# Kernel optimization log

Hardware: AMD Instinct MI355X
Metric: run time of the kernel (lower is better)

The kernel has to match this reference:

```python
import jax, jax.numpy as jnp
import numpy as np

DIM = 256
HEADS = 8
HD = DIM // HEADS        # head_dim = 32
WS = 8                   # window_size (Wh = Ww = 8)
NEXP = 8                 # num_experts
HID = 128                # attr_hidden_size (router hidden)
SCALE = HD ** -0.5


def _window_partition(x, ws):
    # (B, H, W, C) -> (B * H//ws * W//ws, ws, ws, C)
    B, H, W, C = x.shape
    x = x.reshape(B, H // ws, ws, W // ws, ws, C)
    return x.transpose(0, 1, 3, 2, 4, 5).reshape(-1, ws, ws, C)


def _window_reverse(w, ws, B, H, W):
    # inverse of _window_partition
    C = w.shape[-1]
    x = w.reshape(B, H // ws, W // ws, ws, ws, C)
    return x.transpose(0, 1, 3, 2, 4, 5).reshape(B, H, W, C)


def _rope2(x):
    # 2D rotary embedding over a window: x (B*, Wh, Ww, d).
    # First d/2 channels rotated by row position, last d/2 by column position.
    B, Wh, Ww, d = x.shape
    d2 = d // 2

    def angles(L, dd):
        inv = 1.0 / (10000.0 ** (jnp.arange(0, dd, 2, dtype=jnp.float32) / dd))
        return jnp.arange(L, dtype=jnp.float32)[:, None] * inv[None, :]  # (L, dd//2)

    def rotate(v, ang, bshape):
        # v: (B, Wh, Ww, dd) pairs interleaved; ang broadcast as bshape
        p = v.reshape(*v.shape[:-1], -1, 2)
        c = jnp.cos(ang).reshape(bshape)
        s = jnp.sin(ang).reshape(bshape)
        o0 = p[..., 0] * c - p[..., 1] * s
        o1 = p[..., 0] * s + p[..., 1] * c
        return jnp.stack([o0, o1], axis=-1).reshape(v.shape)

    ah = angles(Wh, d2)  # (Wh, d2//2)
    aw = angles(Ww, d2)  # (Ww, d2//2)
    xh = rotate(x[..., :d2], ah, (1, Wh, 1, d2 // 2))
    xw = rotate(x[..., d2:], aw, (1, 1, Ww, d2 // 2))
    return jnp.concatenate([xh, xw], axis=-1)


def _moe_linear(xf, routes, w, b):
    # Top-1 dispatch: per-expert dense GEMM, masked select (jit-safe, static shapes).
    # xf: (T, in), routes: (T,) int, w: (E, out, in), b: (E, out)
    out = jnp.zeros((xf.shape[0], w.shape[1]), xf.dtype)
    for i in range(w.shape[0]):
        y = xf @ w[i].T + b[i]
        out = jnp.where((routes == i)[:, None], y, out)
    return out


def setup_inputs() -> dict:
    key = jax.random.key(0)
    ks = jax.random.split(key, 8)
    sc = 0.02
    return {
        "x": jax.random.normal(ks[0], (8, 64, 64, DIM), jnp.float32),
        "router_w1": jax.random.normal(ks[1], (HID, DIM), jnp.float32) * sc,
        "router_b1": jnp.zeros((HID,), jnp.float32),
        "router_w2": jax.random.normal(ks[2], (NEXP, HID), jnp.float32) * sc,
        "router_b2": jnp.zeros((NEXP,), jnp.float32),
        "qkv_w": jax.random.normal(ks[3], (NEXP, 3 * DIM, DIM), jnp.float32) * sc,
        "qkv_b": jnp.zeros((NEXP, 3 * DIM), jnp.float32),
        "proj_w": jax.random.normal(ks[4], (NEXP, DIM, DIM), jnp.float32) * sc,
        "proj_b": jnp.zeros((NEXP, DIM), jnp.float32),
    }


def reference(x, router_w1, router_b1, router_w2, router_b2,
              qkv_w, qkv_b, proj_w, proj_b):
    Bs, H, W, C = x.shape
    xf = x.reshape(-1, C)  # (T, C), T = Bs*H*W

    # --- Top-1 router (eval mode: no noise, no token dropping) ---
    h = jax.nn.relu(xf @ router_w1.T + router_b1)
    router_logits = h @ router_w2.T + router_b2          # (T, E)
    router_probs = jax.nn.softmax(router_logits, axis=-1)
    route_prob_max = jnp.max(router_probs, axis=-1)       # (T,)
    routes = jnp.argmax(router_probs, axis=-1)            # (T,)

    # --- per-expert QKV projection (grouped dispatch) ---
    qkv = _moe_linear(xf, routes, qkv_w, qkv_b)           # (T, 3C)
    qkv = qkv.reshape(Bs, H, W, 3 * C)

    # --- window partition (shift=0, dilated=1 -> no roll, mask=None) ---
    qw = _window_partition(qkv, WS).reshape(-1, WS * WS, 3 * C)
    B_, N, _ = qw.shape
    qkv5 = qw.reshape(B_, N, 3, HEADS, HD).transpose(2, 0, 3, 1, 4)  # (3,B_,h,N,hd)
    q, k, v = qkv5[0], qkv5[1], qkv5[2]

    # --- RoPE on q, k over the 2D window ---
    q = _rope2(q.reshape(-1, WS, WS, HD)).reshape(B_, HEADS, N, HD)
    k = _rope2(k.reshape(-1, WS, WS, HD)).reshape(B_, HEADS, N, HD)

    # --- windowed attention (moe_mask is all zeros in eval: no drops) ---
    attn = jax.nn.softmax((q * SCALE) @ k.swapaxes(-2, -1), axis=-1)  # (B_,h,N,N)
    out = (attn @ v).swapaxes(1, 2).reshape(B_, N, C)

    # --- window reverse ---
    out = _window_reverse(out.reshape(-1, WS, WS, C), WS, Bs, H, W)

    # --- per-expert output projection + Switch-style prob scaling ---
    of = _moe_linear(out.reshape(-1, C), routes, proj_w, proj_b)
    of = of * route_prob_max[:, None]
    return of.reshape(Bs, H, W, C)
```

## Files before the change

kernel.cpp:

```cpp
#include <hip/hip_runtime.h>
#include <hip/hip_bf16.h>

typedef unsigned short u16;
typedef unsigned int u32;
typedef __attribute__((ext_vector_type(8))) short short8;
typedef __attribute__((ext_vector_type(4))) float f32x4;

#define T_TOK 32768
#define SCALE_ATT 0.17677669529663687f

__device__ __forceinline__ u16 f2bf(float f){
  u32 u = __float_as_uint(f);
  u32 r = u + 0x7fffu + ((u >> 16) & 1u);
  return (u16)(r >> 16);
}
__device__ __forceinline__ float bf2f(u16 h){
  return __uint_as_float(((u32)h) << 16);
}

__global__ void k_cvt(const float* __restrict__ s, u16* __restrict__ d, int n4){
  int i = blockIdx.x * blockDim.x + threadIdx.x;
  if (i < n4){
    float4 v = ((const float4*)s)[i];
    ushort4 o;
    o.x = f2bf(v.x); o.y = f2bf(v.y); o.z = f2bf(v.z); o.w = f2bf(v.w);
    ((ushort4*)d)[i] = o;
  }
}

__global__ void k_cvt_split(const float* __restrict__ s, u16* __restrict__ hi,
                            u16* __restrict__ lo, int n){
  int i = blockIdx.x * blockDim.x + threadIdx.x;
  if (i < n){
    float v = s[i];
    u16 h = f2bf(v);
    hi[i] = h;
    lo[i] = f2bf(v - bf2f(h));
  }
}

__global__ void k_init(int* counts, int* cursors){
  int t = threadIdx.x;
  if (t < 8){ counts[t] = 0; cursors[t] = 0; }
}

__global__ __launch_bounds__(256) void k_router(
    const float* __restrict__ x, const u16* __restrict__ w1h, const u16* __restrict__ w1l,
    const float* __restrict__ b1, const float* __restrict__ w2, const float* __restrict__ b2,
    int* __restrict__ routes, float* __restrict__ pmax, int* __restrict__ counts,
    u16* __restrict__ x_bf)
{
  __shared__ __align__(16) char smem[64*132*4];
  u16* Ah = (u16*)smem;
  u16* Al = Ah + 2560;
  u16* Bh = Al + 2560;
  u16* Bl = Bh + 5120;
  float* Hs = (float*)smem;
  __shared__ int lhist[8];

  int tid = threadIdx.x;
  int t0 = blockIdx.x * 64;
  int wv = tid >> 6, lane = tid & 63, quad = lane >> 4, l16 = lane & 15;
  if (tid < 8) lhist[tid] = 0;

  int arow = tid >> 2, acg = tid & 3;
  int brow = tid >> 1, bhalf = tid & 1;

  f32x4 acc[4][2];
  #pragma unroll
  for (int i = 0; i < 4; ++i)
    #pragma unroll
    for (int j = 0; j < 2; ++j)
      #pragma unroll
      for (int rr = 0; rr < 4; ++rr) acc[i][j][rr] = 0.f;

  for (int kt = 0; kt < 8; ++kt){
    const float* gx = x + (size_t)(t0 + arow) * 256 + kt * 32 + acg * 8;
    float4 v0 = *(const float4*)gx;
    float4 v1 = *(const float4*)(gx + 4);
    ushort4 h0, h1, l0, l1;
    h0.x = f2bf(v0.x); h0.y = f2bf(v0.y); h0.z = f2bf(v0.z); h0.w = f2bf(v0.w);
    h1.x = f2bf(v1.x); h1.y = f2bf(v1.y); h1.z = f2bf(v1.z); h1.w = f2bf(v1.w);
    l0.x = f2bf(v0.x - bf2f(h0.x)); l0.y = f2bf(v0.y - bf2f(h0.y));
    l0.z = f2bf(v0.z - bf2f(h0.z)); l0.w = f2bf(v0.w - bf2f(h0.w));
    l1.x = f2bf(v1.x - bf2f(h1.x)); l1.y = f2bf(v1.y - bf2f(h1.y));
    l1.z = f2bf(v1.z - bf2f(h1.z)); l1.w = f2bf(v1.w - bf2f(h1.w));
    u16* gxb = x_bf + (size_t)(t0 + arow) * 256 + kt * 32 + acg * 8;
    *(ushort4*)gxb = h0; *(ushort4*)(gxb + 4) = h1;
    const u16* gwh = w1h + (size_t)brow * 256 + kt * 32 + bhalf * 16;
    const u16* gwl = w1l + (size_t)brow * 256 + kt * 32 + bhalf * 16;
    uint4 wh0 = *(const uint4*)gwh;
    uint4 wh1 = *(const uint4*)(gwh + 8);
    uint4 wl0 = *(const uint4*)gwl;
    uint4 wl1 = *(const uint4*)(gwl + 8);
    __syncthreads();
    *(ushort4*)&Ah[arow*40 + acg*8    ] = h0;
    *(ushort4*)&Ah[arow*40 + acg*8 + 4] = h1;
    *(ushort4*)&Al[arow*40 + acg*8    ] = l0;
    *(ushort4*)&Al[arow*40 + acg*8 + 4] = l1;
    *(uint4*)&Bh[brow*40 + bhalf*16    ] = wh0;
    *(uint4*)&Bh[brow*40 + bhalf*16 + 8] = wh1;
    *(uint4*)&Bl[brow*40 + bhalf*16    ] = wl0;
    *(uint4*)&Bl[brow*40 + bhalf*16 + 8] = wl1;
    __syncthreads();
    short8 ah[4], al[4], bhf[2], blf[2];
    #pragma unroll
    for (int i = 0; i < 4; ++i){
      ah[i] = *(const short8*)&Ah[(i*16 + l16)*40 + quad*8];
      al[i] = *(const short8*)&Al[(i*16 + l16)*40 + quad*8];
    }
    #pragma unroll
    for (int j = 0; j < 2; ++j){
      bhf[j] = *(const short8*)&Bh[(wv*32 + j*16 + l16)*40 + quad*8];
      blf[j] = *(const short8*)&Bl[(wv*32 + j*16 + l16)*40 + quad*8];
    }
    #pragma unroll
    for (int i = 0; i < 4; ++i)
      #pragma unroll
      for (int j = 0; j < 2; ++j){
        acc[i][j] = __builtin_amdgcn_mfma_f32_16x16x32_bf16(ah[i], bhf[j], acc[i][j], 0, 0, 0);
        acc[i][j] = __builtin_amdgcn_mfma_f32_16x16x32_bf16(ah[i], blf[j], acc[i][j], 0, 0, 0);
        acc[i][j] = __builtin_amdgcn_mfma_f32_16x16x32_bf16(al[i], bhf[j], acc[i][j], 0, 0, 0);
      }
  }
  __syncthreads();

  #pragma unroll
  for (int i = 0; i < 4; ++i)
    #pragma unroll
    for (int j = 0; j < 2; ++j){
      int col = wv*32 + j*16 + l16;
      float bb = b1[col];
      #pragma unroll
      for (int rr = 0; rr < 4; ++rr){
        float h = acc[i][j][rr] + bb;
        Hs[(i*16 + quad*4 + rr)*132 + col] = h > 0.f ? h : 0.f;
      }
    }
  __syncthreads();

  #pragma unroll
  for (int pass = 0; pass < 2; ++pass){
    int mtok = (tid >> 3) + pass * 32;
    int e = tid & 7;
    const float4* w2r = (const float4*)(w2 + e * 128);
    float l = b2[e];
    #pragma unroll
    for (int k4 = 0; k4 < 32; ++k4){
      float4 w = w2r[k4];
      int k = k4 * 4;
      l = fmaf(Hs[mtok*132+k  ], w.x, l);
      l = fmaf(Hs[mtok*132+k+1], w.y, l);
      l = fmaf(Hs[mtok*132+k+2], w.z, l);
      l = fmaf(Hs[mtok*132+k+3], w.w, l);
    }
    float mv = l; int mi = e;
    #pragma unroll
    for (int off = 1; off < 8; off <<= 1){
      float ov = __shfl_xor(mv, off, 64);
      int   oi = __shfl_xor(mi, off, 64);
      if (ov > mv || (ov == mv && oi < mi)){ mv = ov; mi = oi; }
    }
    float sum = expf(l - mv);
    #pragma unroll
    for (int off = 1; off < 8; off <<= 1) sum += __shfl_xor(sum, off, 64);
    if (e == 0){
      int t = t0 + mtok;
      routes[t] = mi;
      pmax[t] = 1.0f / sum;
      atomicAdd(&lhist[mi], 1);
    }
  }
  __syncthreads();
  if (tid < 8 && lhist[tid] > 0) atomicAdd(&counts[tid], lhist[tid]);
}

__global__ void k_offsets(const int* __restrict__ counts, int* __restrict__ offs,
                          int* __restrict__ sorted){
  __shared__ int so[9];
  if (threadIdx.x == 0){
    int o = 0; so[0] = 0;
    for (int e = 0; e < 8; ++e){ o += ((counts[e] + 127) >> 7) << 7; so[e+1] = o; }
    for (int e = 0; e < 9; ++e) offs[e] = so[e];
  }
  __syncthreads();
  for (int e = 0; e < 8; ++e){
    int s = so[e] + counts[e], en = so[e+1];
    for (int i = s + (int)threadIdx.x; i < en; i += (int)blockDim.x) sorted[i] = -1;
  }
}

__global__ __launch_bounds__(256) void k_scatter(
    const int* __restrict__ routes, const int* __restrict__ offs,
    int* __restrict__ cursors, int* __restrict__ sorted, int* __restrict__ rank)
{
  __shared__ int lc[8], lb[8];
  int tid = threadIdx.x;
  int t = blockIdx.x * 256 + tid;
  if (tid < 8) lc[tid] = 0;
  __syncthreads();
  int e = routes[t];
  int rl = atomicAdd(&lc[e], 1);
  __syncthreads();
  if (tid < 8 && lc[tid] > 0) lb[tid] = atomicAdd(&cursors[tid], lc[tid]);
  __syncthreads();
  int pos = offs[e] + lb[e] + rl;
  sorted[pos] = t;
  rank[t] = pos;
}

__global__ __launch_bounds__(256) void k_gather(
    const u16* __restrict__ xbf, const int* __restrict__ sorted,
    const int* __restrict__ offs, u16* __restrict__ xs)
{
  int total = offs[8];
  int tid = threadIdx.x;
  #pragma unroll
  for (int h = 0; h < 2; ++h){
    int cid = tid + h * 256;
    int row = cid >> 5, chunk = cid & 31;
    int gr = blockIdx.x * 16 + row;
    int t = (gr < total) ? sorted[gr] : -1;
    uint4 v = {0u, 0u, 0u, 0u};
    if (t >= 0) v = *(const uint4*)(xbf + (size_t)t * 256 + chunk * 8);
    *(uint4*)(xs + (size_t)gr * 256 + chunk * 8) = v;
  }
}

#define ASTR 56
template<int NOUT, bool PROJ>
__global__ __launch_bounds__(256) void k_gemm(
    const u16* __restrict__ A, const u16* __restrict__ W,
    const float* __restrict__ bias, const int* __restrict__ sidx,
    const int* __restrict__ offs, const float* __restrict__ pmax,
    u16* __restrict__ outb, float* __restrict__ outf)
{
  __shared__ __align__(16) u16 As[128 * ASTR];
  __shared__ __align__(16) u16 Bs[128 * ASTR];
  int tid = threadIdx.x;
  int m0 = blockIdx.y * 128;
  int n0 = blockIdx.x * 128;
  int total = offs[8];
  if (m0 >= total) return;
  int e = 0;
  #pragma unroll
  for (int i = 1; i < 8; ++i) if (m0 >= offs[i]) e = i;

  int wv = tid >> 6, lane = tid & 63, quad = lane >> 4, l16 = lane & 15;
  int wrow = (wv >> 1) * 64, wcol = (wv & 1) * 64;

  int row0 = tid >> 2, c0 = tid & 3;
  const u16* aptr0 = A + (size_t)(m0 + row0) * 256 + c0 * 8;
  const u16* aptr1 = aptr0 + (size_t)64 * 256;
  int pc = (row0 >> 4) + (row0 & 15) * 4;
  const u16* bptr0 = W + ((size_t)e * NOUT + n0 + pc) * 256 + c0 * 8;
  const u16* bptr1 = W + ((size_t)e * NOUT + n0 + 64 + pc) * 256 + c0 * 8;

  f32x4 acc[4][4];
  #pragma unroll
  for (int i = 0; i < 4; ++i)
    #pragma unroll
    for (int j = 0; j < 4; ++j)
      #pragma unroll
      for (int r = 0; r < 4; ++r) acc[i][j][r] = 0.f;

  uint4 a0 = *(const uint4*)aptr0, a1 = *(const uint4*)aptr1;
  uint4 b0 = *(const uint4*)bptr0, b1 = *(const uint4*)bptr1;

  for (int kt = 0; kt < 8; ++kt){
    __syncthreads();
    *(uint4*)&As[ row0      *ASTR + c0*8] = a0;
    *(uint4*)&As[(row0 + 64)*ASTR + c0*8] = a1;
    *(uint4*)&Bs[ row0      *ASTR + c0*8] = b0;
    *(uint4*)&Bs[(row0 + 64)*ASTR + c0*8] = b1;
    __syncthreads();
    if (kt < 7){
      a0 = *(const uint4*)(aptr0 + (kt+1)*32);
      a1 = *(const uint4*)(aptr1 + (kt+1)*32);
      b0 = *(const uint4*)(bptr0 + (kt+1)*32);
      b1 = *(const uint4*)(bptr1 + (kt+1)*32);
    }
    short8 af[4], bfv[4];
    #pragma unroll
    for (int i = 0; i < 4; ++i)
      af[i] = *(const short8*)&As[(wrow + i*16 + l16)*ASTR + quad*8];
    #pragma unroll
    for (int j = 0; j < 4; ++j)
      bfv[j] = *(const short8*)&Bs[(wcol + j*16 + l16)*ASTR + quad*8];
    #pragma unroll
    for (int i = 0; i < 4; ++i)
      #pragma unroll
      for (int j = 0; j < 4; ++j)
        acc[i][j] = __builtin_amdgcn_mfma_f32_16x16x32_bf16(af[i], bfv[j], acc[i][j], 0, 0, 0);
  }

  float4 bj4 = *(const float4*)&bias[e*NOUT + n0 + wcol + l16*4];
  if (PROJ){
    #pragma unroll
    for (int i = 0; i < 4; ++i){
      #pragma unroll
      for (int ri = 0; ri < 4; ++ri){
        int row = wrow + i*16 + quad*4 + ri;
        int t = sidx[m0 + row];
        if (t < 0) continue;
        float pm = pmax[t];
        float4 ov;
        ov.x = (acc[i][0][ri] + bj4.x) * pm;
        ov.y = (acc[i][1][ri] + bj4.y) * pm;
        ov.z = (acc[i][2][ri] + bj4.z) * pm;
        ov.w = (acc[i][3][ri] + bj4.w) * pm;
        *(float4*)&outf[(size_t)t * NOUT + n0 + wcol + l16*4] = ov;
      }
    }
  } else {
    int col0 = n0 + wcol + l16*4;
    bool isqk = (col0 < 512);
    float inv0 = 0.f, inv1 = 0.f;
    float qsc = (col0 < 256) ? SCALE_ATT : 1.0f;
    if (isqk){
      int p0 = (col0 & 15) >> 1;
      inv0 = __expf(-1.1512925465f * (float)p0);
      inv1 = inv0 * 0.31622776601683794f;
    }
    #pragma unroll
    for (int i = 0; i < 4; ++i){
      #pragma unroll
      for (int ri = 0; ri < 4; ++ri){
        int row = wrow + i*16 + quad*4 + ri;
        int t = sidx[m0 + row];
        if (t < 0) continue;
        float vx = acc[i][0][ri] + bj4.x;
        float vy = acc[i][1][ri] + bj4.y;
        float vz = acc[i][2][ri] + bj4.z;
        float vw = acc[i][3][ri] + bj4.w;
        if (isqk){
          float pos = (float)((col0 & 16) ? (t & 7) : ((t >> 6) & 7));
          float a0 = pos * inv0, a1 = pos * inv1;
          float s0, c0s, s1, c1s;
          __sincosf(a0, &s0, &c0s);
          __sincosf(a1, &s1, &c1s);
          float r0 = (vx*c0s - vy*s0) * qsc;
          float r1 = (vx*s0 + vy*c0s) * qsc;
          float r2 = (vz*c1s - vw*s1) * qsc;
          float r3 = (vz*s1 + vw*c1s) * qsc;
          vx = r0; vy = r1; vz = r2; vw = r3;
        }
        uint2 ov;
        ov.x = (u32)f2bf(vx) | ((u32)f2bf(vy) << 16);
        ov.y = (u32)f2bf(vz) | ((u32)f2bf(vw) << 16);
        *(uint2*)&outb[(size_t)t * NOUT + n0 + wcol + l16*4] = ov;
      }
    }
  }
}

__global__ __launch_bounds__(64, 3) void k_attn(const u16* __restrict__ qkv,
                                                const int* __restrict__ rank,
                                                u16* __restrict__ attn_s)
{
  __shared__ __align__(16) u16 Ps[64*72];
  __shared__ __align__(16) u16 Vt[32*72];

  int lane = threadIdx.x;
  int quad = lane >> 4, l16 = lane & 15;
  int wh = blockIdx.x;
  int win = wh >> 3, head = wh & 7;
  int b = win >> 6, wy = (win >> 3) & 7, wx = win & 7;
  int tb = b*4096 + wy*512 + wx*8;

  short8 qf[4], kf[4];
  #pragma unroll
  for (int i = 0; i < 4; ++i){
    int n = i*16 + l16;
    const u16* p = qkv + (size_t)(tb + (n>>3)*64 + (n&7)) * 768 + head*32 + quad*8;
    qf[i] = *(const short8*)p;
    kf[i] = *(const short8*)(p + 256);
  }
  int tn = tb + (lane>>3)*64 + (lane&7);
  const uint4* vb = (const uint4*)(qkv + (size_t)tn * 768 + 512 + head*32);
  uint4 va[4];
  #pragma unroll
  for (int i = 0; i < 4; ++i) va[i] = vb[i];

  f32x4 sa[4][4];
  #pragma unroll
  for (int i = 0; i < 4; ++i)
    #pragma unroll
    for (int j = 0; j < 4; ++j){
      #pragma unroll
      for (int rr = 0; rr < 4; ++rr) sa[i][j][rr] = 0.f;
      sa[i][j] = __builtin_amdgcn_mfma_f32_16x16x32_bf16(qf[i], kf[j], sa[i][j], 0, 0, 0);
    }

  f32x4 rs[4];
  #pragma unroll
  for (int i = 0; i < 4; ++i)
    #pragma unroll
    for (int rr = 0; rr < 4; ++rr){
      float e0 = __expf(sa[i][0][rr]);
      float e1 = __expf(sa[i][1][rr]);
      float e2 = __expf(sa[i][2][rr]);
      float e3 = __expf(sa[i][3][rr]);
      rs[i][rr] = (e0 + e1) + (e2 + e3);
      uint2 pk;
      pk.x = (u32)f2bf(e0) | ((u32)f2bf(e1) << 16);
      pk.y = (u32)f2bf(e2) | ((u32)f2bf(e3) << 16);
      *(uint2*)&Ps[(i*16 + quad*4 + rr)*72 + l16*4] = pk;
    }
  #pragma unroll
  for (int i = 0; i < 4; ++i)
    #pragma unroll
    for (int rr = 0; rr < 4; ++rr){
      #pragma unroll
      for (int off = 1; off < 16; off <<= 1)
        rs[i][rr] += __shfl_xor(rs[i][rr], off, 64);
    }

  u32* vu = (u32*)va;
  int pn = l16 * 4 + quad;
  #pragma unroll
  for (int d2 = 0; d2 < 16; ++d2){
    Vt[(2*d2  )*72 + pn] = (u16)(vu[d2] & 0xffff);
    Vt[(2*d2+1)*72 + pn] = (u16)(vu[d2] >> 16);
  }

  f32x4 oa[4][2];
  #pragma unroll
  for (int i = 0; i < 4; ++i)
    #pragma unroll
    for (int rr = 0; rr < 4; ++rr){ oa[i][0][rr] = 0.f; oa[i][1][rr] = 0.f; }
  #pragma unroll
  for (int ks = 0; ks < 2; ++ks){
    short8 vf0 = *(const short8*)&Vt[(     l16)*72 + ks*32 + quad*8];
    short8 vf1 = *(const short8*)&Vt[(16 + l16)*72 + ks*32 + quad*8];
    #pragma unroll
    for (int i = 0; i < 4; ++i){
      short8 pf = *(const short8*)&Ps[(i*16 + l16)*72 + ks*32 + quad*8];
      oa[i][0] = __builtin_amdgcn_mfma_f32_16x16x32_bf16(pf, vf0, oa[i][0], 0, 0, 0);
      oa[i][1] = __builtin_amdgcn_mfma_f32_16x16x32_bf16(pf, vf1, oa[i][1], 0, 0, 0);
    }
  }

  #pragma unroll
  for (int i = 0; i < 4; ++i)
    #pragma unroll
    for (int rr = 0; rr < 4; ++rr){
      float inv = __builtin_amdgcn_rcpf(rs[i][rr]);
      int m = i*16 + quad*4 + rr;
      int tm = tb + (m >> 3) * 64 + (m & 7);
      int pos = rank[tm];
      u16* op = attn_s + (size_t)pos * 256 + head * 32 + l16;
      op[0]  = f2bf(oa[i][0][rr] * inv);
      op[16] = f2bf(oa[i][1][rr] * inv);
    }
}

extern "C" void kernel_launch(void* const* d_in, const int* in_sizes, int n_in,
                              void* d_out, int out_size, void* d_ws, size_t ws_size,
                              hipStream_t stream){
  const float* x     = (const float*)d_in[0];
  const float* rw1   = (const float*)d_in[1];
  const float* rb1   = (const float*)d_in[2];
  const float* rw2   = (const float*)d_in[3];
  const float* rb2   = (const float*)d_in[4];
  const float* qkvw  = (const float*)d_in[5];
  const float* qkvb  = (const float*)d_in[6];
  const float* projw = (const float*)d_in[7];
  const float* projb = (const float*)d_in[8];
  float* out = (float*)d_out;

  char* ws = (char*)d_ws;
  u16*   x_bf    = (u16*)(ws);
  u16*   qkv_bf  = (u16*)(ws + 16777216);
  u16*   w1h     = (u16*)(ws + 67108864);
  u16*   w1l     = w1h + 32768;
  u16*   xs      = (u16*)(ws + 67108864);
  u16*   attn_s  = (u16*)(ws + 67108864);
  u16*   qw_bf   = (u16*)(ws + 84410368);
  u16*   pw_bf   = (u16*)(ws + 87556096);
  int*   routes  = (int*)(ws + 88604672);
  float* pmaxp   = (float*)(ws + 88735744);
  int*   sorted  = (int*)(ws + 88866816);
  int*   rank    = (int*)(ws + 89001984);
  int*   counts  = (int*)(ws + 89133056);
  int*   cursors = (int*)(ws + 89133056 + 32);
  int*   offs    = (int*)(ws + 89133056 + 64);

  k_init<<<1, 64, 0, stream>>>(counts, cursors);
  k_cvt<<<1536, 256, 0, stream>>>(qkvw,  qw_bf, 1572864/4);
  k_cvt<<< 512, 256, 0, stream>>>(projw, pw_bf,  524288/4);
  k_cvt_split<<<128, 256, 0, stream>>>(rw1, w1h, w1l, 32768);
  k_router<<<512, 256, 0, stream>>>(x, w1h, w1l, rb1, rw2, rb2, routes, pmaxp, counts, x_bf);
  k_offsets<<<1, 256, 0, stream>>>(counts, offs, sorted);
  k_scatter<<<128, 256, 0, stream>>>(routes, offs, cursors, sorted, rank);
  k_gather<<<2112, 256, 0, stream>>>(x_bf, sorted, offs, xs);
  k_gemm<768, false><<<dim3(6, 264), 256, 0, stream>>>(xs, qw_bf, qkvb, sorted, offs,
                                                       nullptr, qkv_bf, nullptr);
  k_attn<<<4096, 64, 0, stream>>>(qkv_bf, rank, attn_s);
  k_gemm<256, true><<<dim3(2, 264), 256, 0, stream>>>(attn_s, pw_bf, projb, sorted, offs,
                                                      pmaxp, nullptr, out);
}
```

Baseline: 224.6 us.

## Fuse prep kernels, fold gather into QKV GEMM, add XCD-aware block swizzle

Merges the weight conversion, split, init and sorted-buffer fill kernels into one prep launch. Folds offset computation into the scatter kernel and removes the gather kernel by having the QKV GEMM load A rows indirectly through the sorted index. Adds an XCD-aware remapping of block IDs in both GEMMs and the attention kernel so neighbouring tiles land on the same chiplet's L2. This cuts launches and an intermediate copy, at the cost of non-contiguous A-row loads inside the GEMM.

```diff
diff --git a/kernel.cpp b/kernel.cpp
--- a/kernel.cpp
+++ b/kernel.cpp
@@ -18,30 +18,42 @@
   return __uint_as_float(((u32)h) << 16);
 }
 
-__global__ void k_cvt(const float* __restrict__ s, u16* __restrict__ d, int n4){
-  int i = blockIdx.x * blockDim.x + threadIdx.x;
-  if (i < n4){
-    float4 v = ((const float4*)s)[i];
+__device__ __forceinline__ int xcd_swz(int flat, int nwg){
+  return (flat & 7) * (nwg >> 3) + (flat >> 3);
+}
+
+__global__ __launch_bounds__(256) void k_prep(
+    const float* __restrict__ qkvw, u16* __restrict__ qw_bf,
+    const float* __restrict__ projw, u16* __restrict__ pw_bf,
+    const float* __restrict__ rw1, u16* __restrict__ w1h, u16* __restrict__ w1l,
+    int* __restrict__ sorted, int* __restrict__ counts, int* __restrict__ cursors)
+{
+  int b = blockIdx.x, tid = threadIdx.x;
+  if (b < 1536){
+    int i = b * 256 + tid;
+    float4 v = ((const float4*)qkvw)[i];
     ushort4 o;
     o.x = f2bf(v.x); o.y = f2bf(v.y); o.z = f2bf(v.z); o.w = f2bf(v.w);
-    ((ushort4*)d)[i] = o;
-  }
-}
-
-__global__ void k_cvt_split(const float* __restrict__ s, u16* __restrict__ hi,
-                            u16* __restrict__ lo, int n){
-  int i = blockIdx.x * blockDim.x + threadIdx.x;
-  if (i < n){
-    float v = s[i];
+    ((ushort4*)qw_bf)[i] = o;
+  } else if (b < 2048){
+    int i = (b - 1536) * 256 + tid;
+    float4 v = ((const float4*)projw)[i];
+    ushort4 o;
+    o.x = f2bf(v.x); o.y = f2bf(v.y); o.z = f2bf(v.z); o.w = f2bf(v.w);
+    ((ushort4*)pw_bf)[i] = o;
+  } else if (b < 2176){
+    int i = (b - 2048) * 256 + tid;
+    float v = rw1[i];
     u16 h = f2bf(v);
-    hi[i] = h;
-    lo[i] = f2bf(v - bf2f(h));
-  }
-}
-
-__global__ void k_init(int* counts, int* cursors){
-  int t = threadIdx.x;
-  if (t < 8){ counts[t] = 0; cursors[t] = 0; }
+    w1h[i] = h;
+    w1l[i] = f2bf(v - bf2f(h));
+  } else if (b < 2209){
+    int i = (b - 2176) * 256 + tid;
+    int4 m1 = {-1, -1, -1, -1};
+    ((int4*)sorted)[i] = m1;
+  } else {
+    if (tid < 8){ counts[tid] = 0; cursors[tid] = 0; }
+  }
 }
 
 __global__ __launch_bounds__(256) void k_router(
@@ -175,60 +187,34 @@
   if (tid < 8 && lhist[tid] > 0) atomicAdd(&counts[tid], lhist[tid]);
 }
 
-__global__ void k_offsets(const int* __restrict__ counts, int* __restrict__ offs,
-                          int* __restrict__ sorted){
-  __shared__ int so[9];
-  if (threadIdx.x == 0){
+__global__ __launch_bounds__(256) void k_scatter(
+    const int* __restrict__ routes, const int* __restrict__ counts,
+    int* __restrict__ cursors, int* __restrict__ sorted, int* __restrict__ rank,
+    int* __restrict__ offs)
+{
+  __shared__ int lc[8], lb[8], so[9];
+  int tid = threadIdx.x;
+  if (tid == 0){
     int o = 0; so[0] = 0;
+    #pragma unroll
     for (int e = 0; e < 8; ++e){ o += ((counts[e] + 127) >> 7) << 7; so[e+1] = o; }
-    for (int e = 0; e < 9; ++e) offs[e] = so[e];
-  }
-  __syncthreads();
-  for (int e = 0; e < 8; ++e){
-    int s = so[e] + counts[e], en = so[e+1];
-    for (int i = s + (int)threadIdx.x; i < en; i += (int)blockDim.x) sorted[i] = -1;
-  }
-}
-
-__global__ __launch_bounds__(256) void k_scatter(
-    const int* __restrict__ routes, const int* __restrict__ offs,
-    int* __restrict__ cursors, int* __restrict__ sorted, int* __restrict__ rank)
-{
-  __shared__ int lc[8], lb[8];
-  int tid = threadIdx.x;
+  }
+  if (tid < 8) lc[tid] = 0;
+  __syncthreads();
   int t = blockIdx.x * 256 + tid;
-  if (tid < 8) lc[tid] = 0;
-  __syncthreads();
   int e = routes[t];
   int rl = atomicAdd(&lc[e], 1);
   __syncthreads();
   if (tid < 8 && lc[tid] > 0) lb[tid] = atomicAdd(&cursors[tid], lc[tid]);
   __syncthreads();
-  int pos = offs[e] + lb[e] + rl;
+  int pos = so[e] + lb[e] + rl;
   sorted[pos] = t;
   rank[t] = pos;
-}
-
-__global__ __launch_bounds__(256) void k_gather(
-    const u16* __restrict__ xbf, const int* __restrict__ sorted,
-    const int* __restrict__ offs, u16* __restrict__ xs)
-{
-  int total = offs[8];
-  int tid = threadIdx.x;
-  #pragma unroll
-  for (int h = 0; h < 2; ++h){
-    int cid = tid + h * 256;
-    int row = cid >> 5, chunk = cid & 31;
-    int gr = blockIdx.x * 16 + row;
-    int t = (gr < total) ? sorted[gr] : -1;
-    uint4 v = {0u, 0u, 0u, 0u};
-    if (t >= 0) v = *(const uint4*)(xbf + (size_t)t * 256 + chunk * 8);
-    *(uint4*)(xs + (size_t)gr * 256 + chunk * 8) = v;
-  }
+  if (blockIdx.x == 0 && tid < 9) offs[tid] = so[tid];
 }
 
 #define ASTR 56
-template<int NOUT, bool PROJ>
+template<int NOUT, bool PROJ, int NB, int NWG>
 __global__ __launch_bounds__(256) void k_gemm(
     const u16* __restrict__ A, const u16* __restrict__ W,
     const float* __restrict__ bias, const int* __restrict__ sidx,
@@ -238,8 +224,10 @@
   __shared__ __align__(16) u16 As[128 * ASTR];
   __shared__ __align__(16) u16 Bs[128 * ASTR];
   int tid = threadIdx.x;
-  int m0 = blockIdx.y * 128;
-  int n0 = blockIdx.x * 128;
+  int flat = blockIdx.y * NB + blockIdx.x;
+  int logical = xcd_swz(flat, NWG);
+  int m0 = (logical / NB) * 128;
+  int n0 = (logical % NB) * 128;
   int total = offs[8];
   if (m0 >= total) return;
   int e = 0;
@@ -250,8 +238,16 @@
   int wrow = (wv >> 1) * 64, wcol = (wv & 1) * 64;
 
   int row0 = tid >> 2, c0 = tid & 3;
-  const u16* aptr0 = A + (size_t)(m0 + row0) * 256 + c0 * 8;
-  const u16* aptr1 = aptr0 + (size_t)64 * 256;
+  const u16 *aptr0, *aptr1;
+  if (PROJ){
+    aptr0 = A + (size_t)(m0 + row0) * 256 + c0 * 8;
+    aptr1 = aptr0 + (size_t)64 * 256;
+  } else {
+    int tA0 = sidx[m0 + row0];      if (tA0 < 0) tA0 = 0;
+    int tA1 = sidx[m0 + row0 + 64]; if (tA1 < 0) tA1 = 0;
+    aptr0 = A + (size_t)tA0 * 256 + c0 * 8;
+    aptr1 = A + (size_t)tA1 * 256 + c0 * 8;
+  }
   int pc = (row0 >> 4) + (row0 & 15) * 4;
   const u16* bptr0 = W + ((size_t)e * NOUT + n0 + pc) * 256 + c0 * 8;
   const u16* bptr1 = W + ((size_t)e * NOUT + n0 + 64 + pc) * 256 + c0 * 8;
@@ -335,10 +331,10 @@
         float vw = acc[i][3][ri] + bj4.w;
         if (isqk){
           float pos = (float)((col0 & 16) ? (t & 7) : ((t >> 6) & 7));
-          float a0 = pos * inv0, a1 = pos * inv1;
+          float a0r = pos * inv0, a1r = pos * inv1;
           float s0, c0s, s1, c1s;
-          __sincosf(a0, &s0, &c0s);
-          __sincosf(a1, &s1, &c1s);
+          __sincosf(a0r, &s0, &c0s);
+          __sincosf(a1r, &s1, &c1s);
           float r0 = (vx*c0s - vy*s0) * qsc;
           float r1 = (vx*s0 + vy*c0s) * qsc;
           float r2 = (vz*c1s - vw*s1) * qsc;
@@ -363,7 +359,7 @@
 
   int lane = threadIdx.x;
   int quad = lane >> 4, l16 = lane & 15;
-  int wh = blockIdx.x;
+  int wh = xcd_swz(blockIdx.x, 4096);
   int win = wh >> 3, head = wh & 7;
   int b = win >> 6, wy = (win >> 3) & 7, wx = win & 7;
   int tb = b*4096 + wy*512 + wx*8;
@@ -474,7 +470,6 @@
   u16*   qkv_bf  = (u16*)(ws + 16777216);
   u16*   w1h     = (u16*)(ws + 67108864);
   u16*   w1l     = w1h + 32768;
-  u16*   xs      = (u16*)(ws + 67108864);
   u16*   attn_s  = (u16*)(ws + 67108864);
   u16*   qw_bf   = (u16*)(ws + 84410368);
   u16*   pw_bf   = (u16*)(ws + 87556096);
@@ -486,17 +481,13 @@
   int*   cursors = (int*)(ws + 89133056 + 32);
   int*   offs    = (int*)(ws + 89133056 + 64);
 
-  k_init<<<1, 64, 0, stream>>>(counts, cursors);
-  k_cvt<<<1536, 256, 0, stream>>>(qkvw,  qw_bf, 1572864/4);
-  k_cvt<<< 512, 256, 0, stream>>>(projw, pw_bf,  524288/4);
-  k_cvt_split<<<128, 256, 0, stream>>>(rw1, w1h, w1l, 32768);
+  k_prep<<<2210, 256, 0, stream>>>(qkvw, qw_bf, projw, pw_bf, rw1, w1h, w1l,
+                                   sorted, counts, cursors);
   k_router<<<512, 256, 0, stream>>>(x, w1h, w1l, rb1, rw2, rb2, routes, pmaxp, counts, x_bf);
-  k_offsets<<<1, 256, 0, stream>>>(counts, offs, sorted);
-  k_scatter<<<128, 256, 0, stream>>>(routes, offs, cursors, sorted, rank);
-  k_gather<<<2112, 256, 0, stream>>>(x_bf, sorted, offs, xs);
-  k_gemm<768, false><<<dim3(6, 264), 256, 0, stream>>>(xs, qw_bf, qkvb, sorted, offs,
-                                                       nullptr, qkv_bf, nullptr);
+  k_scatter<<<128, 256, 0, stream>>>(routes, counts, cursors, sorted, rank, offs);
+  k_gemm<768, false, 6, 1584><<<dim3(6, 264), 256, 0, stream>>>(
+      x_bf, qw_bf, qkvb, sorted, offs, nullptr, qkv_bf, nullptr);
   k_attn<<<4096, 64, 0, stream>>>(qkv_bf, rank, attn_s);
-  k_gemm<256, true><<<dim3(2, 264), 256, 0, stream>>>(attn_s, pw_bf, projb, sorted, offs,
-                                                      pmaxp, nullptr, out);
-}
+  k_gemm<256, true, 2, 528><<<dim3(2, 264), 256, 0, stream>>>(
+      attn_s, pw_bf, projb, sorted, offs, pmaxp, nullptr, out);
+}
```

After: 197.4 us. 1.14x faster.
